# Optimization experiments

Hardware: AMD Instinct MI355X
Metric: run time of the kernel (lower is better)

The kernel has to match this reference:

```python
import jax, jax.numpy as jnp
import numpy as np

N_AUTHOR, N_FOS, N_INST, N_PAPER = 100000, 30000, 8000, 200000
D_IN, D_OUT = 128, 128
# (name, n_src, n_dst, n_edges)
RELS = [("aff", N_AUTHOR, N_INST, 150000), ("ita", N_INST, N_AUTHOR, 150000),
        ("writes", N_AUTHOR, N_PAPER, 500000), ("pta", N_PAPER, N_AUTHOR, 500000),
        ("cites", N_PAPER, N_PAPER, 1000000), ("topic", N_PAPER, N_FOS, 500000),
        ("ftp", N_FOS, N_PAPER, 500000)]
NODE_SIZES = {"author": N_AUTHOR, "fos": N_FOS, "inst": N_INST, "paper": N_PAPER}


def setup_inputs() -> dict:
    key = jax.random.key(0)
    ks = iter(jax.random.split(key, 64))
    inp = {}
    for nt, n in NODE_SIZES.items():
        inp[f"x_{nt}"] = jax.random.normal(next(ks), (n, D_IN), jnp.float32)
    for name, ns, nd, e in RELS:
        inp[f"src_{name}"] = jax.random.randint(next(ks), (e,), 0, ns, jnp.int64)
        inp[f"dst_{name}"] = jax.random.randint(next(ks), (e,), 0, nd, jnp.int64)
    w_scale = 1.0 / np.sqrt(D_IN)
    for nt in NODE_SIZES:
        inp[f"W_root_{nt}"] = jax.random.uniform(next(ks), (D_IN, D_OUT), jnp.float32, -w_scale, w_scale)
        inp[f"b_root_{nt}"] = jax.random.uniform(next(ks), (D_OUT,), jnp.float32, -w_scale, w_scale)
    for name, _, _, _ in RELS:
        inp[f"W_{name}"] = jax.random.uniform(next(ks), (D_IN, D_OUT), jnp.float32, -w_scale, w_scale)
    return inp


def _mean_agg(x_src, src, dst, n_dst):
    # gather source features along edges, mean-reduce into destinations
    msg = x_src[src]                                             # [E, D_IN]
    s = jax.ops.segment_sum(msg, dst, num_segments=n_dst)        # [n_dst, D_IN]
    cnt = jax.ops.segment_sum(jnp.ones_like(dst, dtype=x_src.dtype), dst, num_segments=n_dst)
    return s / jnp.maximum(cnt, 1.0)[:, None]                    # isolated nodes -> 0


def reference(x_author, x_fos, x_inst, x_paper,
              W_root_author, b_root_author, W_root_fos, b_root_fos,
              W_root_inst, b_root_inst, W_root_paper, b_root_paper,
              W_aff, W_ita, W_writes, W_pta, W_cites, W_topic, W_ftp,
              src_aff, dst_aff, src_ita, dst_ita, src_writes, dst_writes,
              src_pta, dst_pta, src_cites, dst_cites, src_topic, dst_topic,
              src_ftp, dst_ftp):
    # root (self) transforms
    out_author = x_author @ W_root_author + b_root_author
    out_fos = x_fos @ W_root_fos + b_root_fos
    out_inst = x_inst @ W_root_inst + b_root_inst
    out_paper = x_paper @ W_root_paper + b_root_paper
    # per-relation aggregate -> linear -> accumulate into destination type
    out_inst = out_inst + _mean_agg(x_author, src_aff, dst_aff, N_INST) @ W_aff
    out_author = out_author + _mean_agg(x_inst, src_ita, dst_ita, N_AUTHOR) @ W_ita
    out_paper = out_paper + _mean_agg(x_author, src_writes, dst_writes, N_PAPER) @ W_writes
    out_author = out_author + _mean_agg(x_paper, src_pta, dst_pta, N_AUTHOR) @ W_pta
    out_paper = out_paper + _mean_agg(x_paper, src_cites, dst_cites, N_PAPER) @ W_cites
    out_fos = out_fos + _mean_agg(x_paper, src_topic, dst_topic, N_FOS) @ W_topic
    out_paper = out_paper + _mean_agg(x_fos, src_ftp, dst_ftp, N_PAPER) @ W_ftp
    # concatenate per-type outputs (author, fos, inst, paper) along node axis
    return jnp.concatenate([out_author, out_fos, out_inst, out_paper], axis=0)
```

## Files before the change

### kernel.cpp

```cpp
#include <hip/hip_runtime.h>

#define N_AUTHOR 100000
#define N_FOS    30000
#define N_INST   8000
#define N_PAPER  200000
#define NCNT     838000
#define ETOT     3300000

#define NBA 1563
#define NBF 469
#define NBI 125
#define NBP 3125
#define NB_TOTAL (NBP + NBA + NBF + NBI)

#define B_AFF    0
#define B_ITA    8000
#define B_WRITES 108000
#define B_PTA    308000
#define B_CITES  408000
#define B_TOPIC  608000
#define B_FTP    638000

typedef __attribute__((ext_vector_type(8))) short short8v;
typedef __attribute__((ext_vector_type(4))) float float4v;
typedef unsigned short us;

__device__ __forceinline__ us f2bf(float f) {
  unsigned u = __float_as_uint(f);
  u = u + 0x7fffu + ((u >> 16) & 1u);
  return (us)(u >> 16);
}
#define BF2F(s) __uint_as_float(((unsigned)(us)(s)) << 16)

__device__ __forceinline__ void acc8(float4v& x, float4v& y, short8v h) {
  x[0] += BF2F(h[0]); x[1] += BF2F(h[1]); x[2] += BF2F(h[2]); x[3] += BF2F(h[3]);
  y[0] += BF2F(h[4]); y[1] += BF2F(h[5]); y[2] += BF2F(h[6]); y[3] += BF2F(h[7]);
}

__device__ __forceinline__ short8v pack8(float4v a, float4v b) {
  short8v h;
  h[0] = (short)f2bf(a[0]); h[1] = (short)f2bf(a[1]);
  h[2] = (short)f2bf(a[2]); h[3] = (short)f2bf(a[3]);
  h[4] = (short)f2bf(b[0]); h[5] = (short)f2bf(b[1]);
  h[6] = (short)f2bf(b[2]); h[7] = (short)f2bf(b[3]);
  return h;
}

#define O_CNT    0
#define O_OFFS   3352000
#define O_CURSOR 6704000
#define O_BTOT   10056000
#define O_CSR    10060096
#define O_WT     23260096
#define XB_AUTHOR 23620544
#define XB_FOS    49220544
#define XB_INST   56900544
#define XB_PAPER  58948544
#define WS_NEED_BF 110148544ULL

struct RelTab { const int* src; const int* dst; int E; int base; };
struct Rels { RelTab r[7]; };
struct WPtrs { const float* w[11]; };
struct XCvt { const float* x; us* xb; int n8; };

__global__ void prep(WPtrs P, us* __restrict__ wt,
                     int* __restrict__ cnt, XCvt x0, XCvt x1, XCvt x2, XCvt x3,
                     Rels R, int doX) {
  int gsz = gridDim.x * blockDim.x;
  int gtid = blockIdx.x * blockDim.x + threadIdx.x;
  for (int i = gtid; i < 11 * 16384; i += gsz) {
    int mat = i >> 14, rem = i & 16383;
    int k = rem >> 7, n = rem & 127;
    wt[mat * 16384 + n * 128 + k] = f2bf(P.w[mat][rem]);
  }
  if (doX) {
    XCvt xc[4] = {x0, x1, x2, x3};
    #pragma unroll
    for (int a = 0; a < 4; ++a) {
      const float* xp = xc[a].x;
      short8v* xbp = (short8v*)xc[a].xb;
      int n8 = xc[a].n8;
      for (int i = gtid; i < n8; i += gsz) {
        float4v v0 = *(const float4v*)(xp + (size_t)i * 8);
        float4v v1 = *(const float4v*)(xp + (size_t)i * 8 + 4);
        xbp[i] = pack8(v0, v1);
      }
    }
  }
  #pragma unroll
  for (int rr = 0; rr < 7; ++rr) {
    const int* dst = R.r[rr].dst;
    int E = R.r[rr].E, base = R.r[rr].base;
    for (int e = gtid; e < E; e += gsz) atomicAdd(&cnt[base + dst[e]], 1);
  }
}

__global__ void scan1(const int* __restrict__ cnt, int* __restrict__ offs,
                      int* __restrict__ btot, int n) {
  __shared__ int sh[256];
  int tid = threadIdx.x;
  int base = blockIdx.x * 2048 + tid * 8;
  int v[8]; int s = 0;
  #pragma unroll
  for (int i = 0; i < 8; ++i) { v[i] = (base + i < n) ? cnt[base + i] : 0; s += v[i]; }
  sh[tid] = s; __syncthreads();
  for (int off = 1; off < 256; off <<= 1) {
    int t = (tid >= off) ? sh[tid - off] : 0;
    __syncthreads();
    sh[tid] += t;
    __syncthreads();
  }
  int excl = sh[tid] - s;
  if (tid == 255) btot[blockIdx.x] = sh[255];
  int run = excl;
  #pragma unroll
  for (int i = 0; i < 8; ++i) { if (base + i < n) offs[base + i] = run; run += v[i]; }
}

__global__ void scan23(int* __restrict__ offs, int* __restrict__ cursor,
                       const int* __restrict__ btot, int nb, int n) {
  __shared__ int sh[512];
  int tid = threadIdx.x;
  int v = (tid < nb) ? btot[tid] : 0;
  sh[tid] = v; __syncthreads();
  for (int off = 1; off < 512; off <<= 1) {
    int t = (tid >= off) ? sh[tid - off] : 0;
    __syncthreads();
    sh[tid] += t;
    __syncthreads();
  }
  int excl = sh[tid] - v;
  __syncthreads();
  sh[tid] = excl;
  __syncthreads();
  int gsz = gridDim.x * 512;
  for (int idx = blockIdx.x * 512 + tid; idx < n; idx += gsz) {
    int val = offs[idx] + sh[idx >> 11];
    offs[idx] = val;
    cursor[idx] = val;
  }
}

__global__ void fill_k(Rels R, int* __restrict__ cursor, int* __restrict__ csr) {
  int gsz = gridDim.x * blockDim.x;
  int gtid = blockIdx.x * blockDim.x + threadIdx.x;
  #pragma unroll
  for (int rr = 0; rr < 7; ++rr) {
    const int* src = R.r[rr].src;
    const int* dst = R.r[rr].dst;
    int E = R.r[rr].E, base = R.r[rr].base;
    for (int e = gtid; e < E; e += gsz) {
      int p = atomicAdd(&cursor[base + dst[e]], 1);
      csr[p] = src[e];
    }
  }
}

template <int NSRC>
__device__ __forceinline__ void fused_body(
    const us* __restrict__ x0, const us* __restrict__ x1,
    const us* __restrict__ x2, const us* __restrict__ x3,
    const us* __restrict__ w0, const us* __restrict__ w1,
    const us* __restrict__ w2, const us* __restrict__ w3,
    int b1, int b2, int b3,
    const int* __restrict__ offs, const int* __restrict__ cnt,
    const int* __restrict__ csr,
    const float* __restrict__ bias, float* __restrict__ out, int n, int rb0) {
  const int lane = threadIdx.x & 63;
  const int wv = threadIdx.x >> 6;
  const int rb = rb0 + wv * 16;
  int ar = rb + (lane & 15); if (ar >= n) ar = n - 1;
  const int cw = (lane >> 4) * 8;

  const us* xs[4] = {x0, x1, x2, x3};
  const us* wsp[4] = {w0, w1, w2, w3};
  const int bases[4] = {0, b1, b2, b3};

  float4v acc[8];
  #pragma unroll
  for (int i = 0; i < 8; ++i) acc[i] = (float4v)0.0f;

  #pragma unroll
  for (int kb = 0; kb < NSRC; ++kb) {
    short8v af[4];
    if (kb == 0) {
      const us* rp = xs[0] + (size_t)ar * 128 + cw;
      #pragma unroll
      for (int ks = 0; ks < 4; ++ks)
        af[ks] = *(const short8v*)(rp + ks * 32);
    } else {
      int gd = bases[kb] + ar;
      int st = offs[gd];
      int deg = cnt[gd];
      const us* xb = xs[kb];
      float4v a0[4], a1[4];
      #pragma unroll
      for (int ks = 0; ks < 4; ++ks) { a0[ks] = (float4v)0.f; a1[ks] = (float4v)0.f; }
      int j = 0;
      for (; j + 2 <= deg; j += 2) {
        int s0 = csr[st + j], s1 = csr[st + j + 1];
        const us* p0 = xb + (size_t)s0 * 128 + cw;
        const us* p1 = xb + (size_t)s1 * 128 + cw;
        #pragma unroll
        for (int ks = 0; ks < 4; ++ks) {
          short8v h0 = *(const short8v*)(p0 + ks * 32);
          short8v h1 = *(const short8v*)(p1 + ks * 32);
          acc8(a0[ks], a1[ks], h0);
          acc8(a0[ks], a1[ks], h1);
        }
      }
      if (j < deg) {
        int s0 = csr[st + j];
        const us* p0 = xb + (size_t)s0 * 128 + cw;
        #pragma unroll
        for (int ks = 0; ks < 4; ++ks) {
          short8v h0 = *(const short8v*)(p0 + ks * 32);
          acc8(a0[ks], a1[ks], h0);
        }
      }
      float sc = 1.0f / (float)((deg > 0) ? deg : 1);
      #pragma unroll
      for (int ks = 0; ks < 4; ++ks)
        af[ks] = pack8(a0[ks] * sc, a1[ks] * sc);
    }
    const us* wb = wsp[kb] + (size_t)(lane & 15) * 128 + cw;
    #pragma unroll
    for (int ct = 0; ct < 8; ++ct) {
      short8v bfr[4];
      #pragma unroll
      for (int ks = 0; ks < 4; ++ks)
        bfr[ks] = *(const short8v*)(wb + ct * 2048 + ks * 32);
      #pragma unroll
      for (int ks = 0; ks < 4; ++ks)
        acc[ct] = __builtin_amdgcn_mfma_f32_16x16x32_bf16(af[ks], bfr[ks], acc[ct], 0, 0, 0);
    }
  }
  #pragma unroll
  for (int ct = 0; ct < 8; ++ct) {
    #pragma unroll
    for (int i = 0; i < 4; ++i) {
      int g = rb + (lane >> 4) * 4 + i;
      if (g < n) {
        int col = ct * 16 + (lane & 15);
        out[(size_t)g * 128 + col] = acc[ct][i] + bias[col];
      }
    }
  }
}

__global__ __launch_bounds__(256, 6) void fused_all(
    const us* __restrict__ xbA, const us* __restrict__ xbF,
    const us* __restrict__ xbI, const us* __restrict__ xbP,
    const us* __restrict__ wt,
    const int* __restrict__ offs, const int* __restrict__ cnt,
    const int* __restrict__ csr,
    const float* __restrict__ bA, const float* __restrict__ bF,
    const float* __restrict__ bI, const float* __restrict__ bP,
    float* __restrict__ out) {
  const int bid = blockIdx.x;
  if (bid < NBP) {
    fused_body<4>(xbP, xbA, xbP, xbF,
                  wt + 3 * 16384, wt + 6 * 16384, wt + 8 * 16384, wt + 10 * 16384,
                  B_WRITES, B_CITES, B_FTP, offs, cnt, csr,
                  bP, out + (size_t)138000 * 128, N_PAPER, bid * 64);
  } else if (bid < NBP + NBA) {
    fused_body<3>(xbA, xbI, xbP, nullptr,
                  wt + 0 * 16384, wt + 5 * 16384, wt + 7 * 16384, nullptr,
                  B_ITA, B_PTA, 0, offs, cnt, csr,
                  bA, out, N_AUTHOR, (bid - NBP) * 64);
  } else if (bid < NBP + NBA + NBF) {
    fused_body<2>(xbF, xbP, nullptr, nullptr,
                  wt + 1 * 16384, wt + 9 * 16384, nullptr, nullptr,
                  B_TOPIC, 0, 0, offs, cnt, csr,
                  bF, out + (size_t)100000 * 128, N_FOS, (bid - NBP - NBA) * 64);
  } else {
    fused_body<2>(xbI, xbA, nullptr, nullptr,
                  wt + 2 * 16384, wt + 4 * 16384, nullptr, nullptr,
                  B_AFF, 0, 0, offs, cnt, csr,
                  bI, out + (size_t)130000 * 128, N_INST, (bid - NBP - NBA - NBF) * 64);
  }
}

typedef float4v f4;
__global__ __launch_bounds__(256, 4) void fb_gemm(
    const float* __restrict__ x0, const float* __restrict__ x1,
    const float* __restrict__ x2, const float* __restrict__ x3,
    const us* __restrict__ w0, const us* __restrict__ w1,
    const us* __restrict__ w2, const us* __restrict__ w3,
    int nsrc, int b1, int b2, int b3,
    const int* __restrict__ offs, const int* __restrict__ cnt,
    const int* __restrict__ csr,
    const float* __restrict__ bias, float* __restrict__ out, int n) {
  const int lane = threadIdx.x & 63;
  const int wv = threadIdx.x >> 6;
  const int rb = blockIdx.x * 64 + wv * 16;
  int ar = rb + (lane & 15); if (ar >= n) ar = n - 1;
  const int cw = (lane >> 4) * 8;
  const float* xs[4] = {x0, x1, x2, x3};
  const us* wsp[4] = {w0, w1, w2, w3};
  const int bases[4] = {0, b1, b2, b3};
  float4v acc[8];
  #pragma unroll
  for (int i = 0; i < 8; ++i) acc[i] = (float4v)0.0f;
  for (int kb = 0; kb < nsrc; ++kb) {
    short8v af[4];
    const float* xb = xs[kb];
    if (kb == 0) {
      const float* rp = xb + (size_t)ar * 128 + cw;
      #pragma unroll
      for (int ks = 0; ks < 4; ++ks) {
        f4 u = *(const f4*)(rp + ks * 32);
        f4 v = *(const f4*)(rp + ks * 32 + 4);
        af[ks] = pack8(u, v);
      }
    } else {
      int gd = bases[kb] + ar;
      int st = offs[gd];
      int deg = cnt[gd];
      f4 a0[4], a1[4];
      #pragma unroll
      for (int ks = 0; ks < 4; ++ks) { a0[ks] = (f4)0.f; a1[ks] = (f4)0.f; }
      for (int j = 0; j < deg; ++j) {
        int s0 = csr[st + j];
        const float* p0 = xb + (size_t)s0 * 128 + cw;
        #pragma unroll
        for (int ks = 0; ks < 4; ++ks) {
          a0[ks] += *(const f4*)(p0 + ks * 32);
          a1[ks] += *(const f4*)(p0 + ks * 32 + 4);
        }
      }
      float sc = 1.0f / (float)((deg > 0) ? deg : 1);
      #pragma unroll
      for (int ks = 0; ks < 4; ++ks)
        af[ks] = pack8(a0[ks] * sc, a1[ks] * sc);
    }
    const us* wb = wsp[kb] + (size_t)(lane & 15) * 128 + cw;
    #pragma unroll
    for (int ct = 0; ct < 8; ++ct) {
      short8v bfr[4];
      #pragma unroll
      for (int ks = 0; ks < 4; ++ks)
        bfr[ks] = *(const short8v*)(wb + ct * 2048 + ks * 32);
      #pragma unroll
      for (int ks = 0; ks < 4; ++ks)
        acc[ct] = __builtin_amdgcn_mfma_f32_16x16x32_bf16(af[ks], bfr[ks], acc[ct], 0, 0, 0);
    }
  }
  #pragma unroll
  for (int ct = 0; ct < 8; ++ct) {
    #pragma unroll
    for (int i = 0; i < 4; ++i) {
      int g = rb + (lane >> 4) * 4 + i;
      if (g < n) {
        int col = ct * 16 + (lane & 15);
        out[(size_t)g * 128 + col] = acc[ct][i] + bias[col];
      }
    }
  }
}

extern "C" void kernel_launch(void* const* d_in, const int* in_sizes, int n_in,
                              void* d_out, int out_size, void* d_ws, size_t ws_size,
                              hipStream_t stream) {
  const float* x_author = (const float*)d_in[0];
  const float* x_fos    = (const float*)d_in[1];
  const float* x_inst   = (const float*)d_in[2];
  const float* x_paper  = (const float*)d_in[3];

  Rels R;
  const int E[7]  = {150000, 150000, 500000, 500000, 1000000, 500000, 500000};
  const int ND[7] = {N_INST, N_AUTHOR, N_PAPER, N_AUTHOR, N_PAPER, N_FOS, N_PAPER};
  int base = 0;
  for (int r = 0; r < 7; ++r) {
    R.r[r].src = (const int*)d_in[4 + 2 * r];
    R.r[r].dst = (const int*)d_in[5 + 2 * r];
    R.r[r].E = E[r];
    R.r[r].base = base;
    base += ND[r];
  }

  char* ws = (char*)d_ws;
  int* cnt    = (int*)(ws + O_CNT);
  int* offs   = (int*)(ws + O_OFFS);
  int* cursor = (int*)(ws + O_CURSOR);
  int* btot   = (int*)(ws + O_BTOT);
  int* csr    = (int*)(ws + O_CSR);
  us* wt  = (us*)(ws + O_WT);
  us* xbA = (us*)(ws + XB_AUTHOR);
  us* xbF = (us*)(ws + XB_FOS);
  us* xbI = (us*)(ws + XB_INST);
  us* xbP = (us*)(ws + XB_PAPER);

  const int useBF = (ws_size >= WS_NEED_BF) ? 1 : 0;

  WPtrs WP;
  WP.w[0] = (const float*)d_in[18];
  WP.w[1] = (const float*)d_in[20];
  WP.w[2] = (const float*)d_in[22];
  WP.w[3] = (const float*)d_in[24];
  for (int r = 0; r < 7; ++r) WP.w[4 + r] = (const float*)d_in[26 + r];

  XCvt xcA = {x_author, xbA, N_AUTHOR * 16};
  XCvt xcF = {x_fos,    xbF, N_FOS * 16};
  XCvt xcI = {x_inst,   xbI, N_INST * 16};
  XCvt xcP = {x_paper,  xbP, N_PAPER * 16};

  hipMemsetAsync(cnt, 0, (size_t)NCNT * 4, stream);
  prep<<<2048, 256, 0, stream>>>(WP, wt, cnt, xcA, xcF, xcI, xcP, R, useBF);
  scan1<<<410, 256, 0, stream>>>(cnt, offs, btot, NCNT);
  scan23<<<1024, 512, 0, stream>>>(offs, cursor, btot, 410, NCNT);
  fill_k<<<2048, 256, 0, stream>>>(R, cursor, csr);

  float* out = (float*)d_out;
  const float* bA = (const float*)d_in[19];
  const float* bF = (const float*)d_in[21];
  const float* bI = (const float*)d_in[23];
  const float* bP = (const float*)d_in[25];

  if (useBF) {
    fused_all<<<NB_TOTAL, 256, 0, stream>>>(xbA, xbF, xbI, xbP, wt,
                                            offs, cnt, csr,
                                            bA, bF, bI, bP, out);
  } else {
    fb_gemm<<<NBA, 256, 0, stream>>>(
        x_author, x_inst, x_paper, nullptr,
        wt + 0 * 16384, wt + 5 * 16384, wt + 7 * 16384, nullptr,
        3, B_ITA, B_PTA, 0, offs, cnt, csr, bA, out, N_AUTHOR);
    fb_gemm<<<NBF, 256, 0, stream>>>(
        x_fos, x_paper, nullptr, nullptr,
        wt + 1 * 16384, wt + 9 * 16384, nullptr, nullptr,
        2, B_TOPIC, 0, 0, offs, cnt, csr, bF, out + (size_t)100000 * 128, N_FOS);
    fb_gemm<<<NBI, 256, 0, stream>>>(
        x_inst, x_author, nullptr, nullptr,
        wt + 2 * 16384, wt + 4 * 16384, nullptr, nullptr,
        2, B_AFF, 0, 0, offs, cnt, csr, bI, out + (size_t)130000 * 128, N_INST);
    fb_gemm<<<NBP, 256, 0, stream>>>(
        x_paper, x_author, x_paper, x_fos,
        wt + 3 * 16384, wt + 6 * 16384, wt + 8 * 16384, wt + 10 * 16384,
        4, B_WRITES, B_CITES, B_FTP, offs, cnt, csr, bP,
        out + (size_t)138000 * 128, N_PAPER);
  }
}
```

Measured before the change: 895.1 us.

## Shard edge count and CSR fill atomics by destination range across block classes

```diff
diff --git a/kernel.cpp b/kernel.cpp
--- a/kernel.cpp
+++ b/kernel.cpp
@@ -6,6 +6,7 @@
 #define N_PAPER  200000
 #define NCNT     838000
 #define ETOT     3300000
+#define NSHARD   (NCNT / 8)
 
 #define NBA 1563
 #define NBF 469
@@ -64,8 +65,7 @@
 struct XCvt { const float* x; us* xb; int n8; };
 
 __global__ void prep(WPtrs P, us* __restrict__ wt,
-                     int* __restrict__ cnt, XCvt x0, XCvt x1, XCvt x2, XCvt x3,
-                     Rels R, int doX) {
+                     XCvt x0, XCvt x1, XCvt x2, XCvt x3, int doX) {
   int gsz = gridDim.x * blockDim.x;
   int gtid = blockIdx.x * blockDim.x + threadIdx.x;
   for (int i = gtid; i < 11 * 16384; i += gsz) {
@@ -87,11 +87,22 @@
       }
     }
   }
+}
+
+__global__ __launch_bounds__(256, 8) void count_sh(Rels R, int* __restrict__ cnt) {
+  const int cls = blockIdx.x & 7;
+  const int lo = cls * NSHARD;
+  const int hi = lo + NSHARD;
+  const int gsz = (gridDim.x >> 3) * 256;
+  const int gtid = (blockIdx.x >> 3) * 256 + threadIdx.x;
   #pragma unroll
   for (int rr = 0; rr < 7; ++rr) {
-    const int* dst = R.r[rr].dst;
-    int E = R.r[rr].E, base = R.r[rr].base;
-    for (int e = gtid; e < E; e += gsz) atomicAdd(&cnt[base + dst[e]], 1);
+    const int* __restrict__ dst = R.r[rr].dst;
+    const int E = R.r[rr].E, base = R.r[rr].base;
+    for (int e = gtid; e < E; e += gsz) {
+      int gd = base + dst[e];
+      if (gd >= lo && gd < hi) atomicAdd(&cnt[gd], 1);
+    }
   }
 }
 
@@ -141,17 +152,24 @@
   }
 }
 
-__global__ void fill_k(Rels R, int* __restrict__ cursor, int* __restrict__ csr) {
-  int gsz = gridDim.x * blockDim.x;
-  int gtid = blockIdx.x * blockDim.x + threadIdx.x;
+__global__ __launch_bounds__(256, 8) void fill_sh(Rels R, int* __restrict__ cursor,
+                                                  int* __restrict__ csr) {
+  const int cls = blockIdx.x & 7;
+  const int lo = cls * NSHARD;
+  const int hi = lo + NSHARD;
+  const int gsz = (gridDim.x >> 3) * 256;
+  const int gtid = (blockIdx.x >> 3) * 256 + threadIdx.x;
   #pragma unroll
   for (int rr = 0; rr < 7; ++rr) {
-    const int* src = R.r[rr].src;
-    const int* dst = R.r[rr].dst;
-    int E = R.r[rr].E, base = R.r[rr].base;
+    const int* __restrict__ src = R.r[rr].src;
+    const int* __restrict__ dst = R.r[rr].dst;
+    const int E = R.r[rr].E, base = R.r[rr].base;
     for (int e = gtid; e < E; e += gsz) {
-      int p = atomicAdd(&cursor[base + dst[e]], 1);
-      csr[p] = src[e];
+      int gd = base + dst[e];
+      if (gd >= lo && gd < hi) {
+        int p = atomicAdd(&cursor[gd], 1);
+        csr[p] = src[e];
+      }
     }
   }
 }
@@ -406,10 +424,11 @@
   XCvt xcP = {x_paper,  xbP, N_PAPER * 16};
 
   hipMemsetAsync(cnt, 0, (size_t)NCNT * 4, stream);
-  prep<<<2048, 256, 0, stream>>>(WP, wt, cnt, xcA, xcF, xcI, xcP, R, useBF);
+  prep<<<2048, 256, 0, stream>>>(WP, wt, xcA, xcF, xcI, xcP, useBF);
+  count_sh<<<2048, 256, 0, stream>>>(R, cnt);
   scan1<<<410, 256, 0, stream>>>(cnt, offs, btot, NCNT);
   scan23<<<1024, 512, 0, stream>>>(offs, cursor, btot, 410, NCNT);
-  fill_k<<<2048, 256, 0, stream>>>(R, cursor, csr);
+  fill_sh<<<2048, 256, 0, stream>>>(R, cursor, csr);
 
   float* out = (float*)d_out;
   const float* bA = (const float*)d_in[19];
```

Measured after the change: 829.0 us. 1.08x faster.
